# Performance work log

Measured on AMD Instinct MI355X. Metric: run time of the kernel, lower is better.

Reference implementation:

```python
import jax, jax.numpy as jnp
import numpy as np

N_NODES = 50000
N_EDGES = 800000
F_IN, F_MID, F_OUT = 256, 128, 40


def gcn_conv(x, W, b, src, dst, n_nodes):
    # GCNConv (PyG defaults): add self-loops, symmetric normalization,
    # linear transform, scatter-sum to targets, then bias.
    h = x @ W  # [N, F_out]
    loop = jnp.arange(n_nodes, dtype=src.dtype)
    s = jnp.concatenate([src, loop])  # sources incl. self-loops
    d = jnp.concatenate([dst, loop])  # targets incl. self-loops
    deg = jax.ops.segment_sum(jnp.ones_like(d, dtype=h.dtype), d, num_segments=n_nodes)
    dinv = jnp.where(deg > 0, jax.lax.rsqrt(deg), 0.0)
    norm = dinv[s] * dinv[d]  # [E+N]
    msgs = h[s] * norm[:, None]  # [E+N, F_out]
    out = jax.ops.segment_sum(msgs, d, num_segments=n_nodes)
    return out + b


def setup_inputs() -> dict:
    key = jax.random.key(0)
    ks = jax.random.split(key, 8)
    x = jax.random.normal(ks[0], (N_NODES, F_IN), dtype=jnp.float32)
    edge_index = jax.random.randint(ks[1], (2, N_EDGES), 0, N_NODES, dtype=jnp.int64)

    def glorot(k, fin, fout):
        lim = float(np.sqrt(6.0 / (fin + fout)))
        return jax.random.uniform(k, (fin, fout), jnp.float32, -lim, lim)

    return {
        "x": x,
        "edge_index": edge_index,
        "W_in": glorot(ks[2], F_IN, F_MID),
        "b_in": jnp.zeros((F_MID,), jnp.float32),
        "W_mid": glorot(ks[3], F_MID, F_MID),
        "b_mid": jnp.zeros((F_MID,), jnp.float32),
        "W_out": glorot(ks[4], F_MID, F_OUT),
        "b_out": jnp.zeros((F_OUT,), jnp.float32),
    }


def reference(x, edge_index, W_in, b_in, W_mid, b_mid, W_out, b_out):
    src, dst = edge_index[0], edge_index[1]
    n = x.shape[0]
    # conv_in -> relu (dropout is identity in eval mode)
    h = jax.nn.relu(gcn_conv(x, W_in, b_in, src, dst, n))
    # middle GCN layer -> relu
    h = jax.nn.relu(gcn_conv(h, W_mid, b_mid, src, dst, n))
    # conv_out -> log_softmax over classes
    h = gcn_conv(h, W_out, b_out, src, dst, n)
    return jax.nn.log_softmax(h, axis=-1)
```

## Files before the change

### kernel.cpp

```cpp
#include <hip/hip_runtime.h>
#include <hip/hip_bf16.h>
#include <math.h>


#define F_IN  256
#define F_MID 128
#define F_OUT 40
#define PSH   9
#define BCAP2 10240

typedef __attribute__((ext_vector_type(8))) short bf16x8;
typedef __attribute__((ext_vector_type(4))) float f32x4;

union FragU {
    bf16x8 v;
    __hip_bfloat162 h2[4];
    uint4 u;
    unsigned short s[8];
};

__device__ __forceinline__ unsigned int f2bf(float f) {
    unsigned int u = __float_as_uint(f);
    return (u + 0x7fffu + ((u >> 16) & 1u)) >> 16;
}
__device__ __forceinline__ float bf_lo(unsigned int u) { return __uint_as_float(u << 16); }
__device__ __forceinline__ float bf_hi(unsigned int u) { return __uint_as_float(u & 0xffff0000u); }

__device__ __forceinline__ void fma_row(float* acc, uint4 u, float d) {
    acc[0] += d * bf_lo(u.x); acc[1] += d * bf_hi(u.x);
    acc[2] += d * bf_lo(u.y); acc[3] += d * bf_hi(u.y);
    acc[4] += d * bf_lo(u.z); acc[5] += d * bf_hi(u.z);
    acc[6] += d * bf_lo(u.w); acc[7] += d * bf_hi(u.w);
}

__global__ __launch_bounds__(256) void k_bucket_prep(const int* __restrict__ src,
                                                     const int* __restrict__ dst,
                                                     unsigned int* __restrict__ bkt,
                                                     int* __restrict__ bcur,
                                                     int E, int nbBkt,
                                                     const float* __restrict__ W1,
                                                     const float* __restrict__ W2,
                                                     const float* __restrict__ W3,
                                                     unsigned short* __restrict__ Wp1,
                                                     unsigned short* __restrict__ Wp2,
                                                     unsigned short* __restrict__ Wp3) {
    if (blockIdx.x >= (unsigned)nbBkt) {
        int t = (blockIdx.x - nbBkt) * 256 + threadIdx.x;
        const float* W; unsigned short* Wp; int M, Mp, kc, nn;
        if (t < 4096)      { W = W1; Wp = Wp1; M = 128; Mp = 128; kc = t >> 7; nn = t & 127; }
        else if (t < 6144) { t -= 4096; W = W2; Wp = Wp2; M = 128; Mp = 128; kc = t >> 7; nn = t & 127; }
        else if (t < 6912) { t -= 6144; W = W3; Wp = Wp3; M = 40;  Mp = 48;  kc = t / 48; nn = t % 48; }
        else return;
        FragU o;
#pragma unroll
        for (int j = 0; j < 8; ++j) {
            int k = kc * 8 + j;
            o.s[j] = (nn < M) ? (unsigned short)f2bf(W[k * M + nn]) : 0;
        }
        *(uint4*)&Wp[((size_t)kc * Mp + nn) * 8] = o.u;
        return;
    }
    __shared__ int hist[128], base[128], cur[128];
    const int t = threadIdx.x;
    if (t < 128) { hist[t] = 0; cur[t] = 0; }
    __syncthreads();
    const int e0 = blockIdx.x * 8192;
    unsigned int mye[32];
#pragma unroll
    for (int j = 0; j < 32; ++j) {
        int e = e0 + j * 256 + t;
        if (e < E) {
            mye[j] = ((unsigned int)dst[e] << 16) | (unsigned int)src[e];
            atomicAdd(&hist[mye[j] >> (16 + PSH)], 1);
        } else mye[j] = 0xffffffffu;
    }
    __syncthreads();
    if (t < 128) base[t] = hist[t] ? atomicAdd(&bcur[t], hist[t]) : 0;
    __syncthreads();
#pragma unroll
    for (int j = 0; j < 32; ++j) {
        if (mye[j] != 0xffffffffu) {
            int p = mye[j] >> (16 + PSH);
            int pos = base[p] + atomicAdd(&cur[p], 1);
            if (pos < BCAP2) bkt[(size_t)p * BCAP2 + pos] = mye[j];
        }
    }
}

__global__ __launch_bounds__(256) void k_gemm1_sort(const unsigned int* __restrict__ bkt,
                                                    const int* __restrict__ bcur,
                                                    int* __restrict__ rofs,
                                                    float* __restrict__ dinv,
                                                    unsigned short* __restrict__ csr,
                                                    int nbG, int npart,
                                                    const float* __restrict__ x,
                                                    const unsigned short* __restrict__ Wp1,
                                                    unsigned short* __restrict__ hn, int n) {
    __shared__ int sh[768];
    if (blockIdx.x >= (unsigned)nbG) {
        int* hist = sh;
        int* stmp = sh + 512;
        const int p = blockIdx.x - nbG;
        const int t = threadIdx.x;
        const int d0 = p << PSH;
        const int nd = min(512, n - d0);

        int bv = (t < p) ? bcur[t] : 0;
        bv = bv > BCAP2 ? BCAP2 : bv;
        stmp[t] = bv;
        hist[t] = 0; hist[t + 256] = 0;
        __syncthreads();
#pragma unroll
        for (int off = 128; off; off >>= 1) {
            if (t < off) stmp[t] += stmp[t + off];
            __syncthreads();
        }
        const int base = stmp[0];
        int np = bcur[p]; np = np > BCAP2 ? BCAP2 : np;
        const unsigned int* b = bkt + (size_t)p * BCAP2;

        for (int i0 = t; i0 < np; i0 += 2048) {
            unsigned int ee[8];
#pragma unroll
            for (int j = 0; j < 8; ++j) {
                int idx = i0 + j * 256;
                ee[j] = (idx < np) ? b[idx] : 0xffffffffu;
            }
#pragma unroll
            for (int j = 0; j < 8; ++j)
                if (ee[j] != 0xffffffffu)
                    atomicAdd(&hist[(int)(ee[j] >> 16) - d0], 1);
        }
        __syncthreads();

        const int h0 = hist[2 * t], h1 = hist[2 * t + 1];
        __syncthreads();
        stmp[t] = h0 + h1;
        __syncthreads();
#pragma unroll
        for (int off = 1; off < 256; off <<= 1) {
            int xx = (t >= off) ? stmp[t - off] : 0;
            __syncthreads();
            stmp[t] += xx;
            __syncthreads();
        }
        const int excl = stmp[t] - (h0 + h1);

        hist[2 * t] = excl;
        hist[2 * t + 1] = excl + h0;
        if (2 * t < nd) {
            rofs[d0 + 2 * t] = base + excl;
            dinv[d0 + 2 * t] = rsqrtf((float)(h0 + 1));
        }
        if (2 * t + 1 < nd) {
            rofs[d0 + 2 * t + 1] = base + excl + h0;
            dinv[d0 + 2 * t + 1] = rsqrtf((float)(h1 + 1));
        }
        if (p == npart - 1 && t == 0) rofs[n] = base + np;
        __syncthreads();

        for (int i0 = t; i0 < np; i0 += 2048) {
            unsigned int ee[8];
#pragma unroll
            for (int j = 0; j < 8; ++j) {
                int idx = i0 + j * 256;
                ee[j] = (idx < np) ? b[idx] : 0xffffffffu;
            }
#pragma unroll
            for (int j = 0; j < 8; ++j) {
                if (ee[j] != 0xffffffffu) {
                    int ld = (int)(ee[j] >> 16) - d0;
                    int pos = atomicAdd(&hist[ld], 1);
                    csr[base + pos] = (unsigned short)(ee[j] & 0xffffu);
                }
            }
        }
        return;
    }
    const int t = threadIdx.x;
    const int w = t >> 6, lane = t & 63, sub = lane & 15, q = lane >> 4;
    const int row0 = blockIdx.x * 64 + w * 16;
    const int row = row0 + sub;
    const bool rv = row < n;
    const float* ap = x + (size_t)row * 256;

    float4 xv[16];
    if (rv) {
#pragma unroll
        for (int j = 0; j < 16; ++j)
            xv[j] = *(const float4*)(ap + (j >> 1) * 32 + q * 8 + (j & 1) * 4);
    } else {
#pragma unroll
        for (int j = 0; j < 16; ++j) xv[j] = make_float4(0.f, 0.f, 0.f, 0.f);
    }

    f32x4 acc[8];
#pragma unroll
    for (int cg = 0; cg < 8; ++cg) acc[cg] = (f32x4)0.f;

#pragma unroll
    for (int kk = 0; kk < 8; ++kk) {
        FragU af;
        float4 f0 = xv[2 * kk];
        float4 f1 = xv[2 * kk + 1];
        af.h2[0] = __float22bfloat162_rn(make_float2(f0.x, f0.y));
        af.h2[1] = __float22bfloat162_rn(make_float2(f0.z, f0.w));
        af.h2[2] = __float22bfloat162_rn(make_float2(f1.x, f1.y));
        af.h2[3] = __float22bfloat162_rn(make_float2(f1.z, f1.w));
        const unsigned short* wrow = Wp1 + (size_t)((kk * 4 + q) * 128 + sub) * 8;
#pragma unroll
        for (int cg = 0; cg < 8; ++cg) {
            bf16x8 b = *(const bf16x8*)(wrow + cg * 16 * 8);
            acc[cg] = __builtin_amdgcn_mfma_f32_16x16x32_bf16(b, af.v, acc[cg], 0, 0, 0);
        }
    }
    if (rv) {
#pragma unroll
        for (int cg = 0; cg < 8; ++cg) {
            uint2 pk;
            pk.x = f2bf(acc[cg][0]) | (f2bf(acc[cg][1]) << 16);
            pk.y = f2bf(acc[cg][2]) | (f2bf(acc[cg][3]) << 16);
            *(uint2*)(hn + (size_t)row * 128 + cg * 16 + q * 4) = pk;
        }
    }
}

template <int MOUT, int MP>
__global__ __launch_bounds__(256) void k_agg_gemm(const unsigned short* __restrict__ hnS,
                                                  const int* __restrict__ rofs,
                                                  const unsigned short* __restrict__ csr,
                                                  const float* __restrict__ dinv,
                                                  const float* __restrict__ bias,
                                                  const unsigned short* __restrict__ Wp,
                                                  unsigned short* __restrict__ hout,
                                                  int n) {
    __shared__ unsigned short arows[16][136];
    const int t = threadIdx.x;
    const int w = t >> 6, lane = t & 63, sub = lane & 15, q = lane >> 4;
    const int v0 = blockIdx.x * 16;
    const int r = w * 4 + q;
    const int node = v0 + r;
    const bool nv = node < n;

    float acc[8];
#pragma unroll
    for (int k = 0; k < 8; ++k) acc[k] = 0.f;

    int e0 = 0, deg = 0;
    if (nv) { e0 = rofs[node]; deg = rofs[node + 1] - e0; }
    const int total = nv ? deg + 1 : 0;
    int ea = (sub < deg) ? (int)csr[e0 + sub] : 0;
    int eb = (16 + sub < deg) ? (int)csr[e0 + 16 + sub] : 0;
    const int lim = (total < 33) ? total : 33;

    for (int ix0 = 0; ix0 < lim; ix0 += 8) {
        int sA[8]; float dA[8];
#pragma unroll
        for (int jj = 0; jj < 8; ++jj) {
            int ix = ix0 + jj;
            int em = (ix - 1) & 15;
            int srcA = __shfl(ea, (lane & 48) + em);
            int srcB = __shfl(eb, (lane & 48) + em);
            int s = (ix - 1 < 16) ? srcA : srcB;
            s = (ix == 0) ? node : s;
            bool ok = ix < lim;
            sA[jj] = ok ? s : 0;
            dA[jj] = ok ? dinv[sA[jj]] : 0.f;
        }
        uint4 u[8];
#pragma unroll
        for (int jj = 0; jj < 8; ++jj)
            u[jj] = *(const uint4*)(hnS + (size_t)sA[jj] * 128 + sub * 8);
#pragma unroll
        for (int jj = 0; jj < 8; ++jj) fma_row(acc, u[jj], dA[jj]);
    }
    for (int ix = 33; ix < total; ++ix) {
        int s = (int)csr[e0 + ix - 1];
        float d = dinv[s];
        uint4 u = *(const uint4*)(hnS + (size_t)s * 128 + sub * 8);
        fma_row(acc, u, d);
    }

    uint4 pk = make_uint4(0, 0, 0, 0);
    if (nv) {
        float dv = dinv[node];
        float4 b0 = *(const float4*)(bias + sub * 8);
        float4 b1 = *(const float4*)(bias + sub * 8 + 4);
        float o0 = fmaxf(dv * acc[0] + b0.x, 0.f);
        float o1 = fmaxf(dv * acc[1] + b0.y, 0.f);
        float o2 = fmaxf(dv * acc[2] + b0.z, 0.f);
        float o3 = fmaxf(dv * acc[3] + b0.w, 0.f);
        float o4 = fmaxf(dv * acc[4] + b1.x, 0.f);
        float o5 = fmaxf(dv * acc[5] + b1.y, 0.f);
        float o6 = fmaxf(dv * acc[6] + b1.z, 0.f);
        float o7 = fmaxf(dv * acc[7] + b1.w, 0.f);
        pk.x = f2bf(o0) | (f2bf(o1) << 16);
        pk.y = f2bf(o2) | (f2bf(o3) << 16);
        pk.z = f2bf(o4) | (f2bf(o5) << 16);
        pk.w = f2bf(o6) | (f2bf(o7) << 16);
    }
    *(uint4*)&arows[r][sub * 8] = pk;
    __syncthreads();

    const int NCG = MP / 16;
    const int NCGW = (MP == 128) ? 2 : 1;
    f32x4 gacc[2];
#pragma unroll
    for (int i = 0; i < 2; ++i) gacc[i] = (f32x4)0.f;

#pragma unroll
    for (int kstep = 0; kstep < 4; ++kstep) {
        FragU af;
        af.u = *(const uint4*)&arows[sub][kstep * 32 + q * 8];
#pragma unroll
        for (int i = 0; i < NCGW; ++i) {
            int cg = w * NCGW + i;
            if (cg < NCG) {
                bf16x8 b = *(const bf16x8*)(Wp + (size_t)((kstep * 4 + q) * MP + cg * 16 + sub) * 8);
                gacc[i] = __builtin_amdgcn_mfma_f32_16x16x32_bf16(b, af.v, gacc[i], 0, 0, 0);
            }
        }
    }
    const int orow = v0 + sub;
    if (orow < n) {
#pragma unroll
        for (int i = 0; i < NCGW; ++i) {
            int cg = w * NCGW + i;
            int feat = cg * 16 + q * 4;
            if (cg < NCG && feat < MOUT) {
                uint2 p2;
                p2.x = f2bf(gacc[i][0]) | (f2bf(gacc[i][1]) << 16);
                p2.y = f2bf(gacc[i][2]) | (f2bf(gacc[i][3]) << 16);
                *(uint2*)(hout + (size_t)orow * MOUT + feat) = p2;
            }
        }
    }
}

__global__ __launch_bounds__(256) void agg40_lsm_bf16(const unsigned short* __restrict__ hnS,
                                                      const int* __restrict__ rofs,
                                                      const unsigned short* __restrict__ csr,
                                                      const float* __restrict__ dinv,
                                                      const float* __restrict__ bias,
                                                      float* __restrict__ out, int n) {
    int wid = (blockIdx.x * 256 + threadIdx.x) >> 6;
    if (wid >= n) return;
    const int v = wid;
    const int lane = threadIdx.x & 63;
    const int h = lane >> 5;
    const int sl = lane & 31;
    const bool act = sl < 20;
    float a0 = 0.f, a1 = 0.f;
    const int e0 = rofs[v];
    const int total = rofs[v + 1] - e0 + 1;

    for (int i0 = 0; i0 < total; i0 += 16) {
        int sA[8];
        unsigned char okA[8];
#pragma unroll
        for (int j = 0; j < 8; ++j) {
            int ix = i0 + h + 2 * j;
            bool ok = ix < total;
            sA[j] = ok ? ((ix == 0) ? v : (int)csr[e0 + ix - 1]) : v;
            okA[j] = ok ? 1 : 0;
        }
        if (act) {
#pragma unroll
            for (int j = 0; j < 8; ++j) {
                float d = okA[j] ? dinv[sA[j]] : 0.f;
                unsigned int u = *(const unsigned int*)(hnS + (size_t)sA[j] * 40 + sl * 2);
                a0 += d * bf_lo(u);
                a1 += d * bf_hi(u);
            }
        }
    }
    a0 += __shfl_xor(a0, 32);
    a1 += __shfl_xor(a1, 32);
    float dv = dinv[v];
    float v0 = act ? (dv * a0 + bias[sl * 2])     : -3.402823466e38f;
    float v1 = act ? (dv * a1 + bias[sl * 2 + 1]) : -3.402823466e38f;
    float m = fmaxf(v0, v1);
#pragma unroll
    for (int off = 16; off; off >>= 1) m = fmaxf(m, __shfl_xor(m, off));
    float p = act ? (__expf(v0 - m) + __expf(v1 - m)) : 0.f;
#pragma unroll
    for (int off = 16; off; off >>= 1) p += __shfl_xor(p, off);
    if (h == 0 && act) {
        float ls = __logf(p);
        *(float2*)(out + (size_t)v * 40 + sl * 2) = make_float2(v0 - m - ls, v1 - m - ls);
    }
}


extern "C" void kernel_launch(void* const* d_in, const int* in_sizes, int n_in,
                              void* d_out, int out_size, void* d_ws, size_t ws_size,
                              hipStream_t stream) {
    const float* x     = (const float*)d_in[0];
    const int*   ei    = (const int*)d_in[1];
    const float* W_in  = (const float*)d_in[2];
    const float* b_in  = (const float*)d_in[3];
    const float* W_mid = (const float*)d_in[4];
    const float* b_mid = (const float*)d_in[5];
    const float* W_out = (const float*)d_in[6];
    const float* b_out = (const float*)d_in[7];
    float* out = (float*)d_out;

    const int N = in_sizes[0] / F_IN;
    const int E = in_sizes[1] / 2;
    const int* srcp = ei;
    const int* dstp = ei + E;
    const int npart = (N + (1 << PSH) - 1) >> PSH;

    char* w = (char*)d_ws;
    unsigned short* hn1 = (unsigned short*)w; w += (size_t)(N + 1) * 128 * 2;
    unsigned short* hn2 = (unsigned short*)w; w += (size_t)(N + 1) * 128 * 2;
    unsigned short* hn3 = (unsigned short*)w; w += (size_t)(N + 1) * 40 * 2 + 16;
    float* dinv = (float*)w; w += (size_t)N * 4;
    int* bcur   = (int*)w;   w += 512;
    int* rofs   = (int*)w;   w += (size_t)(N + 1) * 4 + 12;
    unsigned int* bkt = (unsigned int*)w; w += (size_t)npart * BCAP2 * 4;
    unsigned short* csr = (unsigned short*)w; w += (size_t)E * 2 + 128;
    unsigned short* Wp1 = (unsigned short*)((((size_t)w) + 15) & ~(size_t)15); w = (char*)Wp1 + 32 * 128 * 8 * 2;
    unsigned short* Wp2 = (unsigned short*)w; w += 16 * 128 * 8 * 2;
    unsigned short* Wp3 = (unsigned short*)w; w += 16 * 48 * 8 * 2;

    const int nbW = (N * 64 + 255) / 256;
    const int nbG = (N + 63) / 64;
    const int nbF = (N + 15) / 16;
    const int nbBkt = (E + 8191) / 8192;

    hipMemsetAsync(bcur, 0, 512, stream);
    k_bucket_prep<<<nbBkt + 27, 256, 0, stream>>>(srcp, dstp, bkt, bcur, E, nbBkt,
                                                  W_in, W_mid, W_out, Wp1, Wp2, Wp3);
    k_gemm1_sort<<<nbG + npart, 256, 0, stream>>>(bkt, bcur, rofs, dinv, csr,
                                                  nbG, npart, x, Wp1, hn1, N);
    k_agg_gemm<128, 128><<<nbF, 256, 0, stream>>>(hn1, rofs, csr, dinv, b_in, Wp2, hn2, N);
    k_agg_gemm<40, 48><<<nbF, 256, 0, stream>>>(hn2, rofs, csr, dinv, b_mid, Wp3, hn3, N);
    agg40_lsm_bf16<<<nbW, 256, 0, stream>>>(hn3, rofs, csr, dinv, b_out, out, N);
}
```

Baseline: 230.8 us.

## Prescale layer outputs by source dinv and sub-sort CSR by source range

```diff
diff --git a/kernel.cpp b/kernel.cpp
--- a/kernel.cpp
+++ b/kernel.cpp
@@ -7,6 +7,7 @@
 #define F_MID 128
 #define F_OUT 40
 #define PSH   9
+#define CSH   14
 #define BCAP2 10240
 
 typedef __attribute__((ext_vector_type(8))) short bf16x8;
@@ -31,6 +32,12 @@
     acc[2] += d * bf_lo(u.y); acc[3] += d * bf_hi(u.y);
     acc[4] += d * bf_lo(u.z); acc[5] += d * bf_hi(u.z);
     acc[6] += d * bf_lo(u.w); acc[7] += d * bf_hi(u.w);
+}
+__device__ __forceinline__ void add_row(float* acc, uint4 u) {
+    acc[0] += bf_lo(u.x); acc[1] += bf_hi(u.x);
+    acc[2] += bf_lo(u.y); acc[3] += bf_hi(u.y);
+    acc[4] += bf_lo(u.z); acc[5] += bf_hi(u.z);
+    acc[6] += bf_lo(u.w); acc[7] += bf_hi(u.w);
 }
 
 __global__ __launch_bounds__(256) void k_bucket_prep(const int* __restrict__ src,
@@ -95,20 +102,30 @@
                                                     int nbG, int npart,
                                                     const float* __restrict__ x,
                                                     const unsigned short* __restrict__ Wp1,
-                                                    unsigned short* __restrict__ hn, int n) {
-    __shared__ int sh[768];
+                                                    unsigned short* __restrict__ hn,
+                                                    unsigned short* __restrict__ hn2,
+                                                    unsigned short* __restrict__ hn3,
+                                                    int n) {
+    __shared__ int sh[2304];
     if (blockIdx.x >= (unsigned)nbG) {
         int* hist = sh;
-        int* stmp = sh + 512;
+        int* stmp = sh + 2048;
         const int p = blockIdx.x - nbG;
         const int t = threadIdx.x;
         const int d0 = p << PSH;
         const int nd = min(512, n - d0);
 
+        if (p == 0) {
+            uint4 z = make_uint4(0, 0, 0, 0);
+            if (t < 16) *(uint4*)(hn2 + (size_t)n * 128 + t * 8) = z;
+            else if (t < 21) *(uint4*)(hn3 + (size_t)n * 40 + (t - 16) * 8) = z;
+        }
+
         int bv = (t < p) ? bcur[t] : 0;
         bv = bv > BCAP2 ? BCAP2 : bv;
         stmp[t] = bv;
-        hist[t] = 0; hist[t + 256] = 0;
+#pragma unroll
+        for (int j = 0; j < 8; ++j) hist[t + 256 * j] = 0;
         __syncthreads();
 #pragma unroll
         for (int off = 128; off; off >>= 1) {
@@ -128,14 +145,18 @@
             }
 #pragma unroll
             for (int j = 0; j < 8; ++j)
-                if (ee[j] != 0xffffffffu)
-                    atomicAdd(&hist[(int)(ee[j] >> 16) - d0], 1);
+                if (ee[j] != 0xffffffffu) {
+                    int bin = (((int)(ee[j] >> 16) - d0) << 2) |
+                              ((int)(ee[j] & 0xffffu) >> CSH);
+                    atomicAdd(&hist[bin], 1);
+                }
         }
         __syncthreads();
 
-        const int h0 = hist[2 * t], h1 = hist[2 * t + 1];
-        __syncthreads();
-        stmp[t] = h0 + h1;
+        int h8[8]; int run = 0;
+#pragma unroll
+        for (int j = 0; j < 8; ++j) { h8[j] = hist[t * 8 + j]; run += h8[j]; }
+        stmp[t] = run;
         __syncthreads();
 #pragma unroll
         for (int off = 1; off < 256; off <<= 1) {
@@ -144,17 +165,20 @@
             stmp[t] += xx;
             __syncthreads();
         }
-        const int excl = stmp[t] - (h0 + h1);
-
-        hist[2 * t] = excl;
-        hist[2 * t + 1] = excl + h0;
-        if (2 * t < nd) {
-            rofs[d0 + 2 * t] = base + excl;
-            dinv[d0 + 2 * t] = rsqrtf((float)(h0 + 1));
-        }
-        if (2 * t + 1 < nd) {
-            rofs[d0 + 2 * t + 1] = base + excl + h0;
-            dinv[d0 + 2 * t + 1] = rsqrtf((float)(h1 + 1));
+        int cur = stmp[t] - run;
+#pragma unroll
+        for (int j = 0; j < 8; ++j) { int h = h8[j]; hist[t * 8 + j] = cur; cur += h; }
+        __syncthreads();
+
+#pragma unroll
+        for (int rep = 0; rep < 2; ++rep) {
+            int ld = t + rep * 256;
+            int start = hist[ld * 4];
+            int next = (ld == 511) ? np : hist[ld * 4 + 4];
+            if (ld < nd) {
+                rofs[d0 + ld] = base + start;
+                dinv[d0 + ld] = rsqrtf((float)(next - start + 1));
+            }
         }
         if (p == npart - 1 && t == 0) rofs[n] = base + np;
         __syncthreads();
@@ -169,8 +193,9 @@
 #pragma unroll
             for (int j = 0; j < 8; ++j) {
                 if (ee[j] != 0xffffffffu) {
-                    int ld = (int)(ee[j] >> 16) - d0;
-                    int pos = atomicAdd(&hist[ld], 1);
+                    int bin = (((int)(ee[j] >> 16) - d0) << 2) |
+                              ((int)(ee[j] & 0xffffu) >> CSH);
+                    int pos = atomicAdd(&hist[bin], 1);
                     csr[base + pos] = (unsigned short)(ee[j] & 0xffffu);
                 }
             }
@@ -225,7 +250,7 @@
     }
 }
 
-template <int MOUT, int MP>
+template <int MOUT, int MP, int PRESCALED>
 __global__ __launch_bounds__(256) void k_agg_gemm(const unsigned short* __restrict__ hnS,
                                                   const int* __restrict__ rofs,
                                                   const unsigned short* __restrict__ csr,
@@ -264,21 +289,28 @@
             int s = (ix - 1 < 16) ? srcA : srcB;
             s = (ix == 0) ? node : s;
             bool ok = ix < lim;
-            sA[jj] = ok ? s : 0;
-            dA[jj] = ok ? dinv[sA[jj]] : 0.f;
+            if (PRESCALED) {
+                sA[jj] = ok ? s : n;
+            } else {
+                sA[jj] = ok ? s : 0;
+                dA[jj] = ok ? dinv[sA[jj]] : 0.f;
+            }
         }
         uint4 u[8];
 #pragma unroll
         for (int jj = 0; jj < 8; ++jj)
             u[jj] = *(const uint4*)(hnS + (size_t)sA[jj] * 128 + sub * 8);
 #pragma unroll
-        for (int jj = 0; jj < 8; ++jj) fma_row(acc, u[jj], dA[jj]);
+        for (int jj = 0; jj < 8; ++jj) {
+            if (PRESCALED) add_row(acc, u[jj]);
+            else fma_row(acc, u[jj], dA[jj]);
+        }
     }
     for (int ix = 33; ix < total; ++ix) {
         int s = (int)csr[e0 + ix - 1];
-        float d = dinv[s];
         uint4 u = *(const uint4*)(hnS + (size_t)s * 128 + sub * 8);
-        fma_row(acc, u, d);
+        if (PRESCALED) add_row(acc, u);
+        else fma_row(acc, u, dinv[s]);
     }
 
     uint4 pk = make_uint4(0, 0, 0, 0);
@@ -323,14 +355,15 @@
     }
     const int orow = v0 + sub;
     if (orow < n) {
+        float dvr = dinv[orow];
 #pragma unroll
         for (int i = 0; i < NCGW; ++i) {
             int cg = w * NCGW + i;
             int feat = cg * 16 + q * 4;
             if (cg < NCG && feat < MOUT) {
                 uint2 p2;
-                p2.x = f2bf(gacc[i][0]) | (f2bf(gacc[i][1]) << 16);
-                p2.y = f2bf(gacc[i][2]) | (f2bf(gacc[i][3]) << 16);
+                p2.x = f2bf(dvr * gacc[i][0]) | (f2bf(dvr * gacc[i][1]) << 16);
+                p2.y = f2bf(dvr * gacc[i][2]) | (f2bf(dvr * gacc[i][3]) << 16);
                 *(uint2*)(hout + (size_t)orow * MOUT + feat) = p2;
             }
         }
@@ -356,21 +389,17 @@
 
     for (int i0 = 0; i0 < total; i0 += 16) {
         int sA[8];
-        unsigned char okA[8];
 #pragma unroll
         for (int j = 0; j < 8; ++j) {
             int ix = i0 + h + 2 * j;
-            bool ok = ix < total;
-            sA[j] = ok ? ((ix == 0) ? v : (int)csr[e0 + ix - 1]) : v;
-            okA[j] = ok ? 1 : 0;
+            sA[j] = (ix < total) ? ((ix == 0) ? v : (int)csr[e0 + ix - 1]) : n;
         }
         if (act) {
 #pragma unroll
             for (int j = 0; j < 8; ++j) {
-                float d = okA[j] ? dinv[sA[j]] : 0.f;
                 unsigned int u = *(const unsigned int*)(hnS + (size_t)sA[j] * 40 + sl * 2);
-                a0 += d * bf_lo(u);
-                a1 += d * bf_hi(u);
+                a0 += bf_lo(u);
+                a1 += bf_hi(u);
             }
         }
     }
@@ -433,8 +462,9 @@
     k_bucket_prep<<<nbBkt + 27, 256, 0, stream>>>(srcp, dstp, bkt, bcur, E, nbBkt,
                                                   W_in, W_mid, W_out, Wp1, Wp2, Wp3);
     k_gemm1_sort<<<nbG + npart, 256, 0, stream>>>(bkt, bcur, rofs, dinv, csr,
-                                                  nbG, npart, x, Wp1, hn1, N);
-    k_agg_gemm<128, 128><<<nbF, 256, 0, stream>>>(hn1, rofs, csr, dinv, b_in, Wp2, hn2, N);
-    k_agg_gemm<40, 48><<<nbF, 256, 0, stream>>>(hn2, rofs, csr, dinv, b_mid, Wp3, hn3, N);
+                                                  nbG, npart, x, Wp1, hn1,
+                                                  hn2, hn3, N);
+    k_agg_gemm<128, 128, 0><<<nbF, 256, 0, stream>>>(hn1, rofs, csr, dinv, b_in, Wp2, hn2, N);
+    k_agg_gemm<40, 48, 1><<<nbF, 256, 0, stream>>>(hn2, rofs, csr, dinv, b_mid, Wp3, hn3, N);
     agg40_lsm_bf16<<<nbW, 256, 0, stream>>>(hn3, rofs, csr, dinv, b_out, out, N);
 }
```

Result: faster. 225.8 us (-2.2%).
